# Kernel tuning notes

Hardware: AMD Instinct MI355X
Metric: run time of the kernel (lower is better)

Reference implementation:

```python
import jax, jax.numpy as jnp
import numpy as np

B, LQ, LK, D_WORD, D_K, D_V = 8, 2048, 2048, 1024, 128, 128
TEMPERATURE = 11.313708498984761  # sqrt(d_k)
NEG_BIG = -1e9


def setup_inputs() -> dict:
    key = jax.random.key(0)
    ks = jax.random.split(key, 7)
    scale = 1.0 / np.sqrt(D_WORD)
    return {
        "q": jax.random.normal(ks[0], (B, LQ, D_WORD), dtype=jnp.float32),
        "k": jax.random.normal(ks[1], (B, LK, D_WORD), dtype=jnp.float32),
        "v": jax.random.normal(ks[2], (B, LK, D_WORD), dtype=jnp.float32),
        "memory_lengths": jax.random.randint(ks[3], (B,), 1, LK + 1, dtype=jnp.int32),
        "Wq": jax.random.normal(ks[4], (D_WORD, D_K), dtype=jnp.float32) * scale,
        "Wk": jax.random.normal(ks[5], (D_WORD, D_K), dtype=jnp.float32) * scale,
        "Wv": jax.random.normal(ks[6], (D_WORD, D_V), dtype=jnp.float32) * scale,
    }


def reference(q, k, v, memory_lengths, Wq, Wk, Wv):
    # Projections (bias-free Dense layers)
    qs = jnp.einsum("bqw,wd->bqd", q, Wq)   # [B, LQ, D_K]
    ks = jnp.einsum("bkw,wd->bkd", k, Wk)   # [B, LK, D_K]
    vs = jnp.einsum("bkw,wd->bkd", v, Wv)   # [B, LK, D_V]
    # Scaled dot-product scores
    attn = jnp.einsum("bqd,bkd->bqk", qs, ks) / TEMPERATURE  # [B, LQ, LK]
    # Padding mask from memory_lengths (tf.sequence_mask + tile + where)
    mem_mask = jnp.arange(attn.shape[-1])[None, None, :] < memory_lengths[:, None, None]
    attn = jnp.where(mem_mask, attn, NEG_BIG)
    p = jax.nn.softmax(attn, axis=-1)
    return jnp.einsum("bqk,bkd->bqd", p, vs)  # [B, LQ, D_V]
```

## Files before the change

### kernel.cpp

```cpp
#include <hip/hip_runtime.h>

typedef _Float16 half8 __attribute__((ext_vector_type(8)));
typedef float floatx4 __attribute__((ext_vector_type(4)));

#define INV_TEMP 0.08838834764831845f

#define OFF_WT   0
#define OFF_QS   786432
#define OFF_KT   (786432 + 4194304)
#define OFF_VT   (OFF_KT + 4194304)
#define OFF_PART (OFF_VT + 4194304)
#define PART_BYTES (2ull * 8 * 2048 * 132 * 4)

__global__ __launch_bounds__(256) void wprep_kernel(
    const float* __restrict__ Wq, const float* __restrict__ Wk,
    const float* __restrict__ Wv, _Float16* __restrict__ wt)
{
    __shared__ _Float16 T[64 * 136];
    const int t = threadIdx.x;
    const int kt = blockIdx.x;
    const int m = blockIdx.y;
    const float* W = (m == 0) ? Wq : (m == 1) ? Wk : Wv;
    const float scale = (m == 0) ? INV_TEMP : 1.0f;
    const float* src = W + kt * 8192;

    #pragma unroll
    for (int i = 0; i < 8; i++) {
        int f = i * 1024 + t * 4;
        float4 v = *(const float4*)(src + f);
        int k = f >> 7, n = f & 127;
        _Float16* d = T + k * 136 + n;
        d[0] = (_Float16)(v.x * scale);
        d[1] = (_Float16)(v.y * scale);
        d[2] = (_Float16)(v.z * scale);
        d[3] = (_Float16)(v.w * scale);
    }
    __syncthreads();

    _Float16* dst = wt + m * 131072 + kt * 8192;
    #pragma unroll
    for (int i = 0; i < 4; i++) {
        int p = i * 256 + t;
        int n = p >> 3;
        int c = (p & 7) ^ (n & 7);
        half8 h;
        #pragma unroll
        for (int j = 0; j < 8; j++)
            h[j] = T[(c * 8 + j) * 136 + n];
        *(half8*)(dst + p * 8) = h;
    }
}

__global__ __launch_bounds__(256) void proj_kernel(
    const float* __restrict__ Xq, const float* __restrict__ Xk,
    const float* __restrict__ Xv, const _Float16* __restrict__ wt,
    _Float16* __restrict__ qs, _Float16* __restrict__ ks_t,
    _Float16* __restrict__ vt_t)
{
    __shared__ float As[64 * 128];
    __shared__ _Float16 Bs[2 * 8192];

    const int t = threadIdx.x;
    const int lane = t & 63;
    const int w = t >> 6;
    const int quad = lane >> 4;
    const int m16 = lane & 15;
    const int yb = blockIdx.y;
    const float* X = (yb == 0) ? Xq : (yb == 1) ? Xk : Xv;
    const _Float16* W = wt + yb * 131072;
    const int m0 = blockIdx.x * 64;

    floatx4 acc[8] = {};
    const int e = m16 & 7;

    for (int s = 0; s < 8; s++) {
        if (s) __syncthreads();
        {
            const float* base = X + (size_t)m0 * 1024 + s * 128;
            #pragma unroll
            for (int i = 0; i < 8; i++) {
                int st = i * 256 + t;
                int row = st >> 5;
                int p = st & 31;
                int c = (p & 24) | ((p & 7) ^ (row & 7));
                __builtin_amdgcn_global_load_lds(
                    (const __attribute__((address_space(1))) unsigned int*)(base + (size_t)row * 1024 + c * 4),
                    (__attribute__((address_space(3))) unsigned int*)(As + st * 4),
                    16, 0, 0);
            }
        }
        {
            const _Float16* src = W + s * 16384;
            #pragma unroll
            for (int i = 0; i < 8; i++) {
                int slot = (w * 8 + i) * 64 + lane;
                __builtin_amdgcn_global_load_lds(
                    (const __attribute__((address_space(1))) unsigned int*)(src + (size_t)slot * 8),
                    (__attribute__((address_space(3))) unsigned int*)(Bs + slot * 8),
                    16, 0, 0);
            }
        }
        __builtin_amdgcn_s_waitcnt(0);
        __syncthreads();

        const float* ap = As + (w * 16 + m16) * 128;
        #pragma unroll
        for (int ks = 0; ks < 2; ks++) {
            const char* bt = (const char*)(Bs + ks * 8192);
            #pragma unroll
            for (int hf2 = 0; hf2 < 2; hf2++) {
                int b16 = ks * 16 + hf2 * 8;
                float4 fa = *(const float4*)(ap + (b16 + ((quad * 2) ^ e)) * 4);
                float4 fb = *(const float4*)(ap + (b16 + ((quad * 2 + 1) ^ e)) * 4);
                half8 af = {(_Float16)fa.x, (_Float16)fa.y, (_Float16)fa.z, (_Float16)fa.w,
                            (_Float16)fb.x, (_Float16)fb.y, (_Float16)fb.z, (_Float16)fb.w};
                int sw = (hf2 * 4 + quad) ^ e;
                #pragma unroll
                for (int nt = 0; nt < 8; nt++) {
                    half8 bf = *(const half8*)(bt + (nt * 16 + m16) * 128 + sw * 16);
                    acc[nt] = __builtin_amdgcn_mfma_f32_16x16x32_f16(af, bf, acc[nt], 0, 0, 0);
                }
            }
        }
    }

    const int b = m0 >> 11;
    const int kt = (m0 & 2047) >> 6;

    if (yb == 0) {
        #pragma unroll
        for (int nt = 0; nt < 8; nt++) {
            #pragma unroll
            for (int r = 0; r < 4; r++) {
                int orow = m0 + w * 16 + quad * 4 + r;
                qs[(size_t)orow * 128 + nt * 16 + m16] = (_Float16)acc[nt][r];
            }
        }
    } else if (yb == 1) {
        _Float16* tile = ks_t + (size_t)(b * 32 + kt) * 8192;
        #pragma unroll
        for (int nt = 0; nt < 8; nt++) {
            #pragma unroll
            for (int r = 0; r < 4; r++) {
                int row = w * 16 + quad * 4 + r;
                int col = nt * 16 + m16;
                int p = row * 16 + ((col >> 3) ^ (row & 7));
                tile[p * 8 + (col & 7)] = (_Float16)acc[nt][r];
            }
        }
    } else {
        __syncthreads();
        _Float16* T = (_Float16*)As;
        #pragma unroll
        for (int nt = 0; nt < 8; nt++) {
            #pragma unroll
            for (int r = 0; r < 4; r++)
                T[(w * 16 + quad * 4 + r) * 130 + nt * 16 + m16] = (_Float16)acc[nt][r];
        }
        __syncthreads();
        int dv = t >> 1, hf = t & 1;
        _Float16* tile = vt_t + (size_t)(b * 32 + kt) * 8192;
        #pragma unroll
        for (int j8 = 0; j8 < 4; j8++) {
            int k8 = hf * 4 + j8;
            half8 h;
            #pragma unroll
            for (int j = 0; j < 8; j++)
                h[j] = T[(k8 * 8 + j) * 130 + dv];
            int p = dv * 8 + (k8 ^ (dv & 7));
            *(half8*)(tile + p * 8) = h;
        }
    }
}

__global__ __launch_bounds__(256) void attn_kernel(
    const _Float16* __restrict__ qs, const _Float16* __restrict__ ks_t,
    const _Float16* __restrict__ vt_t, const int* __restrict__ mlen,
    float* __restrict__ out, float* __restrict__ part, int ns)
{
    __shared__ _Float16 kbuf[2 * 8192];
    __shared__ _Float16 vbuf[2 * 8192];
    __shared__ _Float16 pls[4 * 16 * 72];

    const int t = threadIdx.x;
    const int lane = t & 63;
    const int w = t >> 6;
    const int quad = lane >> 4;
    const int m16 = lane & 15;
    const int b = blockIdx.y;
    const int h = blockIdx.z;
    const int q0 = blockIdx.x * 64;
    const int ml = mlen[b];
    const int nkt = (ml + 63) >> 6;
    const int hs = (nkt + ns - 1) / ns;
    const int kb0 = h * hs;
    const int kb1 = min(nkt, (h + 1) * hs);

    half8 aq[4];
    {
        const _Float16* qrow =
            qs + (size_t)(b * 2048 + q0 + w * 16 + m16) * 128 + quad * 8;
        #pragma unroll
        for (int d = 0; d < 4; d++)
            aq[d] = *(const half8*)(qrow + d * 32);
    }

    floatx4 acc[8] = {};
    float m_i[4] = {-3e38f, -3e38f, -3e38f, -3e38f};
    float l_i[4] = {0.f, 0.f, 0.f, 0.f};

    auto stage = [&](int buf, int kt) {
        const _Float16* ksrc = ks_t + (size_t)(b * 32 + kt) * 8192;
        const _Float16* vsrc = vt_t + (size_t)(b * 32 + kt) * 8192;
        #pragma unroll
        for (int i = 0; i < 4; i++) {
            int slot = (w * 4 + i) * 64 + lane;
            __builtin_amdgcn_global_load_lds(
                (const __attribute__((address_space(1))) unsigned int*)(ksrc + (size_t)slot * 8),
                (__attribute__((address_space(3))) unsigned int*)(kbuf + buf * 8192 + slot * 8),
                16, 0, 0);
            __builtin_amdgcn_global_load_lds(
                (const __attribute__((address_space(1))) unsigned int*)(vsrc + (size_t)slot * 8),
                (__attribute__((address_space(3))) unsigned int*)(vbuf + buf * 8192 + slot * 8),
                16, 0, 0);
        }
    };

    if (kb0 < kb1) {
        stage(0, kb0);
        __builtin_amdgcn_s_waitcnt(0);
        __syncthreads();

        for (int kt = kb0; kt < kb1; kt++) {
            const int cur = (kt - kb0) & 1;
            if (kt + 1 < kb1) stage(cur ^ 1, kt + 1);

            const _Float16* kb = kbuf + cur * 8192;
            const _Float16* vb = vbuf + cur * 8192;
            const int k0 = kt * 64;

            floatx4 sacc[4] = {};
            #pragma unroll
            for (int d = 0; d < 4; d++) {
                #pragma unroll
                for (int nt = 0; nt < 4; nt++) {
                    int row = nt * 16 + m16;
                    int p = row * 16 + ((d * 4 + quad) ^ (row & 7));
                    half8 bf = *(const half8*)(kb + p * 8);
                    sacc[nt] = __builtin_amdgcn_mfma_f32_16x16x32_f16(aq[d], bf, sacc[nt], 0, 0, 0);
                }
            }

            float p4[4][4];
            float rowmax[4], rowsum[4];
            #pragma unroll
            for (int r = 0; r < 4; r++) rowmax[r] = -3e38f;
            #pragma unroll
            for (int nt = 0; nt < 4; nt++) {
                int key = k0 + nt * 16 + m16;
                bool valid = key < ml;
                #pragma unroll
                for (int r = 0; r < 4; r++) {
                    float s = valid ? sacc[nt][r] : -3e38f;
                    p4[nt][r] = s;
                    rowmax[r] = fmaxf(rowmax[r], s);
                }
            }
            #pragma unroll
            for (int mask = 8; mask >= 1; mask >>= 1) {
                #pragma unroll
                for (int r = 0; r < 4; r++)
                    rowmax[r] = fmaxf(rowmax[r], __shfl_xor(rowmax[r], mask, 64));
            }
            #pragma unroll
            for (int r = 0; r < 4; r++) {
                float mnew = fmaxf(m_i[r], rowmax[r]);
                float alpha = __expf(m_i[r] - mnew);
                m_i[r] = mnew;
                l_i[r] *= alpha;
                #pragma unroll
                for (int nt = 0; nt < 8; nt++) acc[nt][r] *= alpha;
                rowsum[r] = 0.f;
                #pragma unroll
                for (int nt = 0; nt < 4; nt++) {
                    float ee = __expf(p4[nt][r] - mnew);
                    p4[nt][r] = ee;
                    rowsum[r] += ee;
                }
            }
            #pragma unroll
            for (int mask = 8; mask >= 1; mask >>= 1) {
                #pragma unroll
                for (int r = 0; r < 4; r++)
                    rowsum[r] += __shfl_xor(rowsum[r], mask, 64);
            }
            #pragma unroll
            for (int r = 0; r < 4; r++) l_i[r] += rowsum[r];

            _Float16* pw = pls + w * 16 * 72;
            #pragma unroll
            for (int nt = 0; nt < 4; nt++) {
                #pragma unroll
                for (int r = 0; r < 4; r++)
                    pw[(quad * 4 + r) * 72 + nt * 16 + m16] = (_Float16)p4[nt][r];
            }

            #pragma unroll
            for (int kp = 0; kp < 2; kp++) {
                half8 pa = *(const half8*)(pw + m16 * 72 + kp * 32 + quad * 8);
                #pragma unroll
                for (int nt = 0; nt < 8; nt++) {
                    int dv = nt * 16 + m16;
                    int p = dv * 8 + ((kp * 4 + quad) ^ (dv & 7));
                    half8 bf = *(const half8*)(vb + p * 8);
                    acc[nt] = __builtin_amdgcn_mfma_f32_16x16x32_f16(pa, bf, acc[nt], 0, 0, 0);
                }
            }

            __builtin_amdgcn_s_waitcnt(0);
            __syncthreads();
        }
    }

    if (ns == 1) {
        #pragma unroll
        for (int r = 0; r < 4; r++) {
            float inv_l = 1.0f / l_i[r];
            int orow = b * 2048 + q0 + w * 16 + quad * 4 + r;
            float* dst = out + (size_t)orow * 128;
            #pragma unroll
            for (int nt = 0; nt < 8; nt++)
                dst[nt * 16 + m16] = acc[nt][r] * inv_l;
        }
    } else {
        #pragma unroll
        for (int r = 0; r < 4; r++) {
            float* pr = part +
                (size_t)(h * 16384 + b * 2048 + q0 + w * 16 + quad * 4 + r) * 132;
            #pragma unroll
            for (int nt = 0; nt < 8; nt++)
                pr[nt * 16 + m16] = acc[nt][r];
            if (m16 == 0) { pr[128] = m_i[r]; pr[129] = l_i[r]; }
        }
    }
}

__global__ __launch_bounds__(256) void merge_kernel(
    const float* __restrict__ part, float* __restrict__ out)
{
    int idx = blockIdx.x * 256 + threadIdx.x;
    int row = idx >> 7, c = idx & 127;
    const float* p1 = part + (size_t)row * 132;
    const float* p2 = part + (size_t)(16384 + row) * 132;
    float m1 = p1[128], l1 = p1[129];
    float m2 = p2[128], l2 = p2[129];
    float M = fmaxf(m1, m2);
    float s1 = __expf(m1 - M), s2 = __expf(m2 - M);
    out[idx] = (p1[c] * s1 + p2[c] * s2) / (l1 * s1 + l2 * s2);
}

extern "C" void kernel_launch(void* const* d_in, const int* in_sizes, int n_in,
                              void* d_out, int out_size, void* d_ws, size_t ws_size,
                              hipStream_t stream) {
    const float* q   = (const float*)d_in[0];
    const float* k   = (const float*)d_in[1];
    const float* v   = (const float*)d_in[2];
    const int* mlen  = (const int*)d_in[3];
    const float* Wq  = (const float*)d_in[4];
    const float* Wk  = (const float*)d_in[5];
    const float* Wv  = (const float*)d_in[6];
    float* out = (float*)d_out;

    char* ws = (char*)d_ws;
    _Float16* wt   = (_Float16*)(ws + OFF_WT);
    _Float16* qs   = (_Float16*)(ws + OFF_QS);
    _Float16* ks_t = (_Float16*)(ws + OFF_KT);
    _Float16* vt_t = (_Float16*)(ws + OFF_VT);
    float* part    = (float*)(ws + OFF_PART);

    const int ns = (ws_size >= (size_t)OFF_PART + PART_BYTES) ? 2 : 1;

    hipLaunchKernelGGL(wprep_kernel, dim3(16, 3), dim3(256), 0, stream, Wq, Wk, Wv, wt);
    hipLaunchKernelGGL(proj_kernel, dim3(256, 3), dim3(256), 0, stream,
                       q, k, v, wt, qs, ks_t, vt_t);
    hipLaunchKernelGGL(attn_kernel, dim3(32, 8, ns), dim3(256), 0, stream,
                       qs, ks_t, vt_t, mlen, out, part, ns);
    if (ns == 2)
        hipLaunchKernelGGL(merge_kernel, dim3(8192), dim3(256), 0, stream, part, out);
}
```

Baseline: 260.2 us.

## Double-buffer projection GEMM K-slices to overlap global loads with MFMA

The projection kernel now splits K into 16 slices of 64 instead of 8 slices of 128, and keeps two LDS buffers. The next slice's async global-to-LDS loads are issued before computing on the current one, with a partial vmcnt wait. This is meant to hide global memory latency behind the MFMA work, at the cost of twice as many barriers and tighter reliance on the hand-written waitcnt counts.

```diff
diff --git a/kernel.cpp b/kernel.cpp
--- a/kernel.cpp
+++ b/kernel.cpp
@@ -57,8 +57,8 @@
     _Float16* __restrict__ qs, _Float16* __restrict__ ks_t,
     _Float16* __restrict__ vt_t)
 {
-    __shared__ float As[64 * 128];
-    __shared__ _Float16 Bs[2 * 8192];
+    __shared__ float As[2][64 * 64];
+    __shared__ _Float16 Bs[2][8192];
 
     const int t = threadIdx.x;
     const int lane = t & 63;
@@ -73,55 +73,66 @@
     floatx4 acc[8] = {};
     const int e = m16 & 7;
 
-    for (int s = 0; s < 8; s++) {
-        if (s) __syncthreads();
+    auto stage = [&](int buf, int s) {
         {
-            const float* base = X + (size_t)m0 * 1024 + s * 128;
-            #pragma unroll
-            for (int i = 0; i < 8; i++) {
+            const float* base = X + (size_t)m0 * 1024 + s * 64;
+            #pragma unroll
+            for (int i = 0; i < 4; i++) {
                 int st = i * 256 + t;
-                int row = st >> 5;
-                int p = st & 31;
-                int c = (p & 24) | ((p & 7) ^ (row & 7));
+                int row = st >> 4;
+                int p = st & 15;
+                int c = (p & 8) | ((p & 7) ^ (row & 7));
                 __builtin_amdgcn_global_load_lds(
                     (const __attribute__((address_space(1))) unsigned int*)(base + (size_t)row * 1024 + c * 4),
-                    (__attribute__((address_space(3))) unsigned int*)(As + st * 4),
+                    (__attribute__((address_space(3))) unsigned int*)(&As[buf][st * 4]),
                     16, 0, 0);
             }
         }
         {
-            const _Float16* src = W + s * 16384;
-            #pragma unroll
-            for (int i = 0; i < 8; i++) {
-                int slot = (w * 8 + i) * 64 + lane;
+            const _Float16* src = W + s * 8192;
+            #pragma unroll
+            for (int i = 0; i < 4; i++) {
+                int slot = (w * 4 + i) * 64 + lane;
                 __builtin_amdgcn_global_load_lds(
                     (const __attribute__((address_space(1))) unsigned int*)(src + (size_t)slot * 8),
-                    (__attribute__((address_space(3))) unsigned int*)(Bs + slot * 8),
+                    (__attribute__((address_space(3))) unsigned int*)(&Bs[buf][slot * 8]),
                     16, 0, 0);
             }
         }
-        __builtin_amdgcn_s_waitcnt(0);
-        __syncthreads();
-
-        const float* ap = As + (w * 16 + m16) * 128;
-        #pragma unroll
-        for (int ks = 0; ks < 2; ks++) {
-            const char* bt = (const char*)(Bs + ks * 8192);
-            #pragma unroll
-            for (int hf2 = 0; hf2 < 2; hf2++) {
-                int b16 = ks * 16 + hf2 * 8;
-                float4 fa = *(const float4*)(ap + (b16 + ((quad * 2) ^ e)) * 4);
-                float4 fb = *(const float4*)(ap + (b16 + ((quad * 2 + 1) ^ e)) * 4);
-                half8 af = {(_Float16)fa.x, (_Float16)fa.y, (_Float16)fa.z, (_Float16)fa.w,
-                            (_Float16)fb.x, (_Float16)fb.y, (_Float16)fb.z, (_Float16)fb.w};
-                int sw = (hf2 * 4 + quad) ^ e;
-                #pragma unroll
-                for (int nt = 0; nt < 8; nt++) {
-                    half8 bf = *(const half8*)(bt + (nt * 16 + m16) * 128 + sw * 16);
-                    acc[nt] = __builtin_amdgcn_mfma_f32_16x16x32_f16(af, bf, acc[nt], 0, 0, 0);
-                }
-            }
-        }
+    };
+
+    stage(0, 0);
+
+    for (int s = 0; s < 16; s++) {
+        const int cur = s & 1;
+        if (s + 1 < 16) {
+            stage(cur ^ 1, s + 1);
+            asm volatile("s_waitcnt vmcnt(8)" ::: "memory");
+        } else {
+            asm volatile("s_waitcnt vmcnt(0)" ::: "memory");
+        }
+        __builtin_amdgcn_s_barrier();
+        asm volatile("" ::: "memory");
+
+        const float* ap = &As[cur][(w * 16 + m16) * 64];
+        const char* bt = (const char*)&Bs[cur][0];
+        #pragma unroll
+        for (int hf2 = 0; hf2 < 2; hf2++) {
+            float4 fa = *(const float4*)(ap + (hf2 * 8 + ((quad * 2) ^ e)) * 4);
+            float4 fb = *(const float4*)(ap + (hf2 * 8 + ((quad * 2 + 1) ^ e)) * 4);
+            half8 af = {(_Float16)fa.x, (_Float16)fa.y, (_Float16)fa.z, (_Float16)fa.w,
+                        (_Float16)fb.x, (_Float16)fb.y, (_Float16)fb.z, (_Float16)fb.w};
+            int sw = (hf2 * 4 + quad) ^ e;
+            #pragma unroll
+            for (int nt = 0; nt < 8; nt++) {
+                half8 bf = *(const half8*)(bt + (nt * 16 + m16) * 128 + sw * 16);
+                acc[nt] = __builtin_amdgcn_mfma_f32_16x16x32_f16(af, bf, acc[nt], 0, 0, 0);
+            }
+        }
+
+        asm volatile("" ::: "memory");
+        __builtin_amdgcn_s_barrier();
+        asm volatile("" ::: "memory");
     }
 
     const int b = m0 >> 11;
```

Measured after the change: 264.2 us. About the same (+1.6%).

## Stage full fp16 X row tile in LDS before projection MFMA loop

Applied to the files above, without the earlier changes.

The projection kernel now loads the whole 64x1024 activation tile up front through registers. It converts it to fp16 and stores it swizzled in LDS, so the fp32 staging and the per-fragment conversion inside the MFMA loop go away. The main loop then streams only 64-wide weight chunks over 16 steps, and launch bounds now allow one block per CU. The cost is about 144KB of LDS per block, which cuts occupancy, and the large upfront activation load no longer overlaps with compute.

```diff
diff --git a/kernel.cpp b/kernel.cpp
--- a/kernel.cpp
+++ b/kernel.cpp
@@ -1,6 +1,7 @@
 #include <hip/hip_runtime.h>
 
 typedef _Float16 half8 __attribute__((ext_vector_type(8)));
+typedef _Float16 half4v __attribute__((ext_vector_type(4)));
 typedef float floatx4 __attribute__((ext_vector_type(4)));
 
 #define INV_TEMP 0.08838834764831845f
@@ -51,14 +52,14 @@
     }
 }
 
-__global__ __launch_bounds__(256) void proj_kernel(
+__global__ __launch_bounds__(256, 1) void proj_kernel(
     const float* __restrict__ Xq, const float* __restrict__ Xk,
     const float* __restrict__ Xv, const _Float16* __restrict__ wt,
     _Float16* __restrict__ qs, _Float16* __restrict__ ks_t,
     _Float16* __restrict__ vt_t)
 {
-    __shared__ float As[64 * 128];
-    __shared__ _Float16 Bs[2 * 8192];
+    __shared__ _Float16 Af[64 * 1024];
+    __shared__ _Float16 Bs[8192];
 
     const int t = threadIdx.x;
     const int lane = t & 63;
@@ -71,29 +72,48 @@
     const int m0 = blockIdx.x * 64;
 
     floatx4 acc[8] = {};
-    const int e = m16 & 7;
-
-    for (int s = 0; s < 8; s++) {
-        if (s) __syncthreads();
+
+    {
+        const float* src = X + (size_t)m0 * 1024;
+        const int ch = t >> 1;
+        const int half = (t & 1) * 4;
+        #pragma unroll
+        for (int g = 0; g < 8; g++) {
+            float4 c0, c1, c2, c3, c4, c5, c6, c7;
+            const float* s0 = src + (size_t)(g * 8) * 1024 + t * 4;
+            c0 = *(const float4*)(s0);
+            c1 = *(const float4*)(s0 + 1024);
+            c2 = *(const float4*)(s0 + 2048);
+            c3 = *(const float4*)(s0 + 3072);
+            c4 = *(const float4*)(s0 + 4096);
+            c5 = *(const float4*)(s0 + 5120);
+            c6 = *(const float4*)(s0 + 6144);
+            c7 = *(const float4*)(s0 + 7168);
+            #pragma unroll
+            for (int j = 0; j < 8; j++) {
+                float4 c = (j == 0) ? c0 : (j == 1) ? c1 : (j == 2) ? c2 :
+                           (j == 3) ? c3 : (j == 4) ? c4 : (j == 5) ? c5 :
+                           (j == 6) ? c6 : c7;
+                int row = g * 8 + j;
+                int chp = (ch & ~7) | ((ch & 7) ^ (row & 7));
+                half4v h = {(_Float16)c.x, (_Float16)c.y,
+                            (_Float16)c.z, (_Float16)c.w};
+                *(half4v*)(Af + row * 1024 + chp * 8 + half) = h;
+            }
+        }
+    }
+    __syncthreads();
+
+    const int rm = w * 16 + m16;
+    const int e = rm & 7;
+    const _Float16* arow = Af + rm * 1024;
+
+    for (int s = 0; s < 16; s++) {
         {
-            const float* base = X + (size_t)m0 * 1024 + s * 128;
-            #pragma unroll
-            for (int i = 0; i < 8; i++) {
-                int st = i * 256 + t;
-                int row = st >> 5;
-                int p = st & 31;
-                int c = (p & 24) | ((p & 7) ^ (row & 7));
-                __builtin_amdgcn_global_load_lds(
-                    (const __attribute__((address_space(1))) unsigned int*)(base + (size_t)row * 1024 + c * 4),
-                    (__attribute__((address_space(3))) unsigned int*)(As + st * 4),
-                    16, 0, 0);
-            }
-        }
-        {
-            const _Float16* src = W + s * 16384;
-            #pragma unroll
-            for (int i = 0; i < 8; i++) {
-                int slot = (w * 8 + i) * 64 + lane;
+            const _Float16* src = W + s * 8192;
+            #pragma unroll
+            for (int i = 0; i < 4; i++) {
+                int slot = (w * 4 + i) * 64 + lane;
                 __builtin_amdgcn_global_load_lds(
                     (const __attribute__((address_space(1))) unsigned int*)(src + (size_t)slot * 8),
                     (__attribute__((address_space(3))) unsigned int*)(Bs + slot * 8),
@@ -103,25 +123,18 @@
         __builtin_amdgcn_s_waitcnt(0);
         __syncthreads();
 
-        const float* ap = As + (w * 16 + m16) * 128;
-        #pragma unroll
-        for (int ks = 0; ks < 2; ks++) {
-            const char* bt = (const char*)(Bs + ks * 8192);
-            #pragma unroll
-            for (int hf2 = 0; hf2 < 2; hf2++) {
-                int b16 = ks * 16 + hf2 * 8;
-                float4 fa = *(const float4*)(ap + (b16 + ((quad * 2) ^ e)) * 4);
-                float4 fb = *(const float4*)(ap + (b16 + ((quad * 2 + 1) ^ e)) * 4);
-                half8 af = {(_Float16)fa.x, (_Float16)fa.y, (_Float16)fa.z, (_Float16)fa.w,
-                            (_Float16)fb.x, (_Float16)fb.y, (_Float16)fb.z, (_Float16)fb.w};
-                int sw = (hf2 * 4 + quad) ^ e;
-                #pragma unroll
-                for (int nt = 0; nt < 8; nt++) {
-                    half8 bf = *(const half8*)(bt + (nt * 16 + m16) * 128 + sw * 16);
-                    acc[nt] = __builtin_amdgcn_mfma_f32_16x16x32_f16(af, bf, acc[nt], 0, 0, 0);
-                }
-            }
-        }
+        #pragma unroll
+        for (int hf2 = 0; hf2 < 2; hf2++) {
+            int chp = s * 8 + ((hf2 * 4 + quad) ^ e);
+            half8 af = *(const half8*)(arow + chp * 8);
+            int sw = (hf2 * 4 + quad) ^ e;
+            #pragma unroll
+            for (int nt = 0; nt < 8; nt++) {
+                half8 bf = *(const half8*)((const char*)Bs + (nt * 16 + m16) * 128 + sw * 16);
+                acc[nt] = __builtin_amdgcn_mfma_f32_16x16x32_f16(af, bf, acc[nt], 0, 0, 0);
+            }
+        }
+        __syncthreads();
     }
 
     const int b = m0 >> 11;
@@ -149,8 +162,7 @@
             }
         }
     } else {
-        __syncthreads();
-        _Float16* T = (_Float16*)As;
+        _Float16* T = Af;
         #pragma unroll
         for (int nt = 0; nt < 8; nt++) {
             #pragma unroll
```

Measured after the change: 290.6 us. +11.7%, slower.
